# Kernel optimization log

Hardware: AMD Instinct MI355X
Metric: run time of the kernel (lower is better)

## Reference

```python
import jax, jax.numpy as jnp
import numpy as np

NBIT = 8
NSPLIT = 255.0  # 2**NBIT - 1


def _quantized_matmul(x, w_clean, eps):
    # Faithful port of quantization(): bit-slice x into NBIT binary planes, run a
    # noisy linear per plane with weight w + randn*|w|*0.1, and sum. The 8
    # sequential fc() calls are fused into one einsum over the bit axis.
    # x: (..., in); w_clean: (out, in); eps: (NBIT, out, in) standard normal.
    mn = jnp.min(x)
    mx = jnp.max(x)
    q = ((x - mn) / (mx - mn) * NSPLIT).astype(jnp.uint8).astype(jnp.int32)  # truncating cast as in torch
    quant_base = 2 ** jnp.arange(NBIT, dtype=jnp.int32)
    binary = ((q[..., None] & quant_base) != 0).astype(x.dtype)              # (..., in, NBIT)
    scaled = binary * (2.0 ** jnp.arange(NBIT)).astype(x.dtype)              # plane i scaled by 2**i
    w_noisy = w_clean[None] + eps * jnp.abs(w_clean)[None] * 0.1             # (NBIT, out, in)
    z = jnp.einsum('...ib,boi->...o', scaled, w_noisy)
    return z, mn, mx, w_noisy[-1]  # fc.weight after loop == last noisy weight


def _forward(node_embedding, edge_embedding, nbr_mask, cond1, cond2, eps1, eps2, bn_gamma, bn_beta):
    B, At, Nbr, Fe = edge_embedding.shape
    Fn = node_embedding.shape[-1]
    c1 = jnp.concatenate(
        [jnp.broadcast_to(node_embedding[:, :, None, :], (B, At, Nbr, Fn)), edge_embedding],
        axis=3)                                                              # (B, At, Nbr, Fn+Fe)
    # quantization + re_quantization through fc (re-quant uses last noisy fc.weight)
    z1, mn1, mx1, w_last = _quantized_matmul(c1, cond1[0], eps1)
    bias1 = jnp.sum(mn1 * w_last, axis=1)                                    # (H1,)
    h = jax.nn.relu(z1 / NSPLIT * (mx1 - mn1) + bias1)                       # (B, At, Nbr, H1)
    # quantization + re_quantization through fc_2 (re-quant uses conductance[1][-1])
    z2, mn2, mx2, _ = _quantized_matmul(h, cond2[0], eps2)
    bias2 = jnp.sum(mn2 * cond2[-1], axis=1)                                 # (2*Fn,)
    c2 = z2 / NSPLIT * (mx2 - mn2) + bias2                                   # (B, At, Nbr, 2*Fn)
    nbr_gate, nbr_extract = jnp.split(c2, 2, axis=3)
    nbr_sumed = jax.nn.sigmoid(nbr_gate) * jnp.tanh(nbr_extract) * nbr_mask[..., None]
    nbr_sumed = jnp.sum(nbr_sumed, axis=2)                                   # (B, At, Fn)
    # BatchNorm1d in training mode: batch statistics over flattened (B*At)
    flat = nbr_sumed.reshape(-1, Fn)
    mean = jnp.mean(flat, axis=0)
    var = jnp.var(flat, axis=0)  # biased variance, as torch BN uses for normalization
    bn = ((flat - mean) / jnp.sqrt(var + 1e-5) * bn_gamma + bn_beta).reshape(B, At, Fn)
    return jax.nn.relu(node_embedding + bn)


def setup_inputs() -> dict:
    key = jax.random.key(0)
    ks = jax.random.split(key, 7)
    B, At, Nbr, Fn, Fe = 16, 96, 12, 64, 64
    H1, H2 = 4 * (Fn + Fe), 2 * Fn
    return {
        'node_embedding': jax.random.normal(ks[0], (B, At, Fn), jnp.float32),
        'edge_embedding': jax.random.normal(ks[1], (B, At, Nbr, Fe), jnp.float32),
        'nbr_mask': (jax.random.uniform(ks[2], (B, At, Nbr)) > 0.5).astype(jnp.float32),
        'cond1': jax.random.normal(ks[3], (2, H1, Fn + Fe), jnp.float32) * 0.05,
        'cond2': jax.random.normal(ks[4], (2, H2, H1), jnp.float32) * 0.05,
        'eps1': jax.random.normal(ks[5], (NBIT, H1, Fn + Fe), jnp.float32),
        'eps2': jax.random.normal(ks[6], (NBIT, H2, H1), jnp.float32),
        'bn_gamma': jnp.ones((Fn,), jnp.float32),
        'bn_beta': jnp.zeros((Fn,), jnp.float32),
    }


def reference(node_embedding, edge_embedding, nbr_mask, cond1, cond2, eps1, eps2, bn_gamma, bn_beta):
    return _forward(node_embedding, edge_embedding, nbr_mask, cond1, cond2, eps1, eps2, bn_gamma, bn_beta)
```

## Files before the change

### kernel.cpp

```cpp
#include <hip/hip_runtime.h>
#include <stdint.h>

#define B_    16
#define AT_   96
#define NBR_  12
#define FN_   64
#define FE_   64
#define M1    (B_*AT_*NBR_)
#define R_    (B_*AT_)
#define K1Q   128
#define N1    512
#define K2Q   512
#define N2    128
#define SPLIT2 4

typedef _Float16 f16x8 __attribute__((ext_vector_type(8)));
typedef _Float16 f16x2 __attribute__((ext_vector_type(2)));
typedef float    f32x4 __attribute__((ext_vector_type(4)));

#define OFF_SCAL  0u
#define OFF_B1R   256u
#define OFF_B2R   (OFF_B1R + 2048u)
#define OFF_Q1    4096u
#define OFF_W1E   (OFF_Q1  + (size_t)M1*K1Q)
#define OFF_W2E   (OFF_W1E + (size_t)N1*K1Q*8*2)
#define OFF_Q2    (OFF_W2E + (size_t)N2*K2Q*8*2)
#define OFF_H     (OFF_Q2  + (size_t)M1*K2Q)
#define OFF_ZP    OFF_H
#define OFF_NS    (OFF_H   + (size_t)M1*N1*2)

__device__ __forceinline__ unsigned int enc_f(float f) {
    unsigned int u = __float_as_uint(f);
    return (u & 0x80000000u) ? ~u : (u | 0x80000000u);
}
__device__ __forceinline__ float dec_f(unsigned int u) {
    return __uint_as_float((u & 0x80000000u) ? (u & 0x7FFFFFFFu) : ~u);
}

__global__ void k_init(unsigned int* scal, float* b1raw, float* b2raw) {
    int t = threadIdx.x;
    if (t == 0) { scal[0] = 0xFFFFFFFFu; scal[1] = 0u; scal[2] = 0xFFFFFFFFu; scal[3] = 0u; }
    if (t < N1) b1raw[t] = 0.f;
    if (t < N2) b2raw[t] = 0.f;
}

__global__ __launch_bounds__(256) void k_minmax_c1(const float* __restrict__ node,
                                                   const float* __restrict__ edge,
                                                   unsigned int* __restrict__ scal) {
    const int nn4 = (B_*AT_*FN_)/4;
    const int tot4 = nn4 + (M1*FE_)/4;
    float mn = 3.0e38f, mx = -3.0e38f;
    for (int idx = blockIdx.x*blockDim.x + threadIdx.x; idx < tot4; idx += gridDim.x*blockDim.x) {
        float4 x = (idx < nn4) ? ((const float4*)node)[idx] : ((const float4*)edge)[idx - nn4];
        mn = fminf(mn, fminf(fminf(x.x, x.y), fminf(x.z, x.w)));
        mx = fmaxf(mx, fmaxf(fmaxf(x.x, x.y), fmaxf(x.z, x.w)));
    }
    __shared__ float smn[256], smx[256];
    smn[threadIdx.x] = mn; smx[threadIdx.x] = mx; __syncthreads();
    for (int s = 128; s > 0; s >>= 1) {
        if (threadIdx.x < s) {
            smn[threadIdx.x] = fminf(smn[threadIdx.x], smn[threadIdx.x+s]);
            smx[threadIdx.x] = fmaxf(smx[threadIdx.x], smx[threadIdx.x+s]);
        }
        __syncthreads();
    }
    if (threadIdx.x == 0) { atomicMin(&scal[0], enc_f(smn[0])); atomicMax(&scal[1], enc_f(smx[0])); }
}

template<int KQ, int N, int SBASE, bool USE_SECOND>
__global__ __launch_bounds__(256) void k_prep_w16(const float* __restrict__ w_clean,
                                                  const float* __restrict__ eps,
                                                  const unsigned int* __restrict__ scal,
                                                  float* __restrict__ braw,
                                                  _Float16* __restrict__ We) {
    int idx = blockIdx.x*blockDim.x + threadIdx.x;
    if (idx >= N*KQ) return;
    int o = idx / KQ;
    float mn = dec_f(scal[SBASE]), mx = dec_f(scal[SBASE+1]);
    float s = (mx - mn) * (1.0f/255.0f);
    float w = w_clean[idx];
    float aw = fabsf(w) * 0.1f;
    union { _Float16 h[8]; uint4 u; } pk;
    float p = s;
    float v7 = 0.f;
    #pragma unroll
    for (int b = 0; b < 8; b++) {
        float e = eps[(size_t)b*N*KQ + idx];
        float v = w + e*aw;
        if (b == 7) v7 = v;
        pk.h[b] = (_Float16)(v * p);
        p *= 2.0f;
    }
    *(uint4*)&We[(size_t)idx*8] = pk.u;
    float bv = USE_SECOND ? w_clean[(size_t)N*KQ + idx] : v7;
    #pragma unroll
    for (int off = 32; off > 0; off >>= 1) bv += __shfl_down(bv, off);
    if ((threadIdx.x & 63) == 0) atomicAdd(&braw[o], bv);
}

__global__ __launch_bounds__(256) void k_quant_c1(const float* __restrict__ node,
                                                  const float* __restrict__ edge,
                                                  const unsigned int* __restrict__ scal,
                                                  unsigned int* __restrict__ q1) {
    int idx = blockIdx.x*256 + threadIdx.x;
    int m = idx >> 5, dw = idx & 31;
    const float mn = dec_f(scal[0]), rng = dec_f(scal[1]) - mn;
    float4 x;
    if (dw < 16) x = *(const float4*)&node[(m/NBR_)*FN_ + dw*4];
    else         x = *(const float4*)&edge[(size_t)m*FE_ + (dw-16)*4];
    unsigned int b0 = (unsigned char)(int)((x.x - mn) / rng * 255.0f);
    unsigned int b1 = (unsigned char)(int)((x.y - mn) / rng * 255.0f);
    unsigned int b2 = (unsigned char)(int)((x.z - mn) / rng * 255.0f);
    unsigned int b3 = (unsigned char)(int)((x.w - mn) / rng * 255.0f);
    q1[idx] = b0 | (b1 << 8) | (b2 << 16) | (b3 << 24);
}

__global__ __launch_bounds__(256) void k_quant_h(const _Float16* __restrict__ h,
                                                 const unsigned int* __restrict__ scal,
                                                 unsigned int* __restrict__ q2) {
    int idx = blockIdx.x*256 + threadIdx.x;
    const float mn = dec_f(scal[2]), rng = dec_f(scal[3]) - mn;
    f16x8 v = *(const f16x8*)(h + (size_t)idx*8);
    unsigned int lo = 0, hi = 0;
    #pragma unroll
    for (int j = 0; j < 4; j++) {
        float x = (float)v[j];
        lo |= ((unsigned int)(unsigned char)(int)((x - mn) / rng * 255.0f)) << (j*8);
    }
    #pragma unroll
    for (int j = 0; j < 4; j++) {
        float x = (float)v[4+j];
        hi |= ((unsigned int)(unsigned char)(int)((x - mn) / rng * 255.0f)) << (j*8);
    }
    uint2 o; o.x = lo; o.y = hi;
    *(uint2*)&q2[idx*2] = o;
}

__device__ __forceinline__ f16x8 expand_byte(unsigned int byte) {
    unsigned int r2 = byte | (byte << 15);
    union { unsigned int u[4]; f16x8 h; } t;
    t.u[0] = ( r2       & 0x00010001u) * 0x3C00u;
    t.u[1] = ((r2 >> 2) & 0x00010001u) * 0x3C00u;
    t.u[2] = ((r2 >> 4) & 0x00010001u) * 0x3C00u;
    t.u[3] = ((r2 >> 6) & 0x00010001u) * 0x3C00u;
    return t.h;
}

template<int KQ, int N, int SPLITK, bool EPI1>
__global__ __launch_bounds__(256, 3) void kge(const unsigned char* __restrict__ q,
                                              const _Float16* __restrict__ W,
                                              const float* __restrict__ braw,
                                              void* __restrict__ outv,
                                              unsigned int* __restrict__ scal) {
    constexpr int KP  = KQ * 8;
    constexpr int KPS = KP / SPLITK;
    constexpr int NIT = KPS / 64;
    __shared__ __align__(16) unsigned char ldsA[4*64*136];

    const int tid  = threadIdx.x;
    const int lane = tid & 63;
    const int w    = tid >> 6;
    const int l15  = lane & 15;
    const int lq   = lane >> 4;
    const int sh8  = lq * 8;
    const int m0   = blockIdx.x * 256 + w * 64;
    const int o0   = blockIdx.y * 64;
    const int kbase = blockIdx.z * KPS;

    unsigned char* wlds = ldsA + w * (64*136);

    {
        const int rsub = lane >> 3;
        const int c    = lane & 7;
        const unsigned int koff = (unsigned int)(kbase >> 3);
        #pragma unroll
        for (int j = 0; j < 8; ++j) {
            const int row = j*8 + rsub;
            uint4 v = *(const uint4*)(q + (size_t)(m0 + row)*KQ + koff + c*16);
            unsigned char* dst = wlds + row*136 + c*16;
            uint2 lo; lo.x = v.x; lo.y = v.y;
            uint2 hi; hi.x = v.z; hi.y = v.w;
            *(uint2*)dst = lo;
            *(uint2*)(dst + 8) = hi;
        }
    }

    f32x4 acc[4][4] = {};

    unsigned int boff[8];
    #pragma unroll
    for (int nf = 0; nf < 4; ++nf)
        #pragma unroll
        for (int kf = 0; kf < 2; ++kf)
            boff[nf*2+kf] = (unsigned int)(o0 + nf*16 + l15) * KP + kbase + kf*32 + lq*8;

    f16x8 bf0[8], bf1[8];
    #pragma unroll
    for (int j = 0; j < 8; ++j)
        bf0[j] = *(const f16x8*)(W + boff[j]);

    const unsigned char* ards = wlds + l15*136;

    #pragma unroll 2
    for (int it = 0; it < NIT; ++it) {
        const f16x8* cur = (it & 1) ? bf1 : bf0;
        f16x8*       nxt = (it & 1) ? bf0 : bf1;
        if (it + 1 < NIT) {
            #pragma unroll
            for (int j = 0; j < 8; ++j)
                nxt[j] = *(const f16x8*)(W + boff[j] + (it+1)*64);
        }
        uint2 qd[4];
        #pragma unroll
        for (int mf = 0; mf < 4; ++mf)
            qd[mf] = *(const uint2*)(ards + mf*(16*136) + it*8);
        #pragma unroll
        for (int kf = 0; kf < 2; ++kf) {
            #pragma unroll
            for (int mf = 0; mf < 4; ++mf) {
                unsigned int byte = ((kf ? qd[mf].y : qd[mf].x) >> sh8) & 0xFFu;
                f16x8 a = expand_byte(byte);
                #pragma unroll
                for (int nf = 0; nf < 4; ++nf)
                    acc[mf][nf] = __builtin_amdgcn_mfma_f32_16x16x32_f16(a, cur[nf*2+kf], acc[mf][nf], 0, 0, 0);
            }
        }
    }

    if (EPI1) {
        _Float16* out = (_Float16*)outv;
        const float mn1 = dec_f(scal[0]);
        float bv[4];
        #pragma unroll
        for (int nf = 0; nf < 4; ++nf) bv[nf] = mn1 * braw[o0 + nf*16 + l15];
        float tmn = 3.0e38f, tmx = -3.0e38f;
        #pragma unroll
        for (int mf = 0; mf < 4; ++mf) {
            const int mr = m0 + mf*16 + lq*4;
            #pragma unroll
            for (int nf = 0; nf < 4; ++nf) {
                const int oc = o0 + nf*16 + l15;
                #pragma unroll
                for (int r = 0; r < 4; ++r) {
                    float v = fmaxf(acc[mf][nf][r] + bv[nf], 0.0f);
                    _Float16 v16 = (_Float16)v;
                    float vr = (float)v16;
                    tmn = fminf(tmn, vr); tmx = fmaxf(tmx, vr);
                    out[(size_t)(mr + r)*N + oc] = v16;
                }
            }
        }
        float* red = (float*)ldsA;
        __syncthreads();
        red[tid] = tmn; red[256 + tid] = tmx;
        __syncthreads();
        for (int s = 128; s > 0; s >>= 1) {
            if (tid < s) {
                red[tid]       = fminf(red[tid],       red[tid + s]);
                red[256 + tid] = fmaxf(red[256 + tid], red[256 + tid + s]);
            }
            __syncthreads();
        }
        if (tid == 0) { atomicMin(&scal[2], enc_f(red[0])); atomicMax(&scal[3], enc_f(red[256])); }
    } else {
        _Float16* op = (_Float16*)outv + (size_t)blockIdx.z * ((size_t)M1 * N);
        #pragma unroll
        for (int mf = 0; mf < 4; ++mf) {
            const int mr = m0 + mf*16 + lq*4;
            #pragma unroll
            for (int nf = 0; nf < 4; ++nf) {
                const int oc = o0 + nf*16 + l15;
                #pragma unroll
                for (int r = 0; r < 4; ++r)
                    op[(size_t)(mr + r)*N + oc] = (_Float16)acc[mf][nf][r];
            }
        }
    }
}

__global__ __launch_bounds__(256) void k_nbr(const _Float16* __restrict__ zp,
                                             const float* __restrict__ b2raw,
                                             const unsigned int* __restrict__ scal,
                                             const float* __restrict__ mask,
                                             float* __restrict__ ns) {
    const size_t SP = (size_t)M1 * N2;
    int tid = threadIdx.x;
    int r = blockIdx.x*8 + (tid >> 5);
    int f2 = (tid & 31) * 2;
    const float mn2 = dec_f(scal[2]);
    float bg0 = mn2 * b2raw[f2],      bg1 = mn2 * b2raw[f2+1];
    float be0 = mn2 * b2raw[64 + f2], be1 = mn2 * b2raw[65 + f2];
    float s0 = 0.f, s1 = 0.f;
    #pragma unroll
    for (int n = 0; n < NBR_; n++) {
        int m = r*NBR_ + n;
        size_t base = (size_t)m * N2;
        float g0 = bg0, g1 = bg1, e0 = be0, e1 = be1;
        #pragma unroll
        for (int z = 0; z < SPLIT2; z++) {
            f16x2 gv = *(const f16x2*)(zp + z*SP + base + f2);
            f16x2 ev = *(const f16x2*)(zp + z*SP + base + 64 + f2);
            g0 += (float)gv[0]; g1 += (float)gv[1];
            e0 += (float)ev[0]; e1 += (float)ev[1];
        }
        float mk = mask[m];
        s0 += (1.0f / (1.0f + expf(-g0))) * tanhf(e0) * mk;
        s1 += (1.0f / (1.0f + expf(-g1))) * tanhf(e1) * mk;
    }
    float2 o; o.x = s0; o.y = s1;
    *(float2*)&ns[r*64 + f2] = o;
}

__global__ __launch_bounds__(256) void k_bn(const float* __restrict__ ns,
                                            const float* __restrict__ node,
                                            const float* __restrict__ gamma,
                                            const float* __restrict__ beta,
                                            float* __restrict__ out) {
    int f = blockIdx.x;
    int tid = threadIdx.x;
    float x[6];
    float s = 0.f, ss = 0.f;
    #pragma unroll
    for (int k = 0; k < 6; k++) {
        int r = tid + k*256;
        x[k] = ns[r*64 + f];
        s += x[k]; ss += x[k]*x[k];
    }
    __shared__ float rs[256], rss[256];
    rs[tid] = s; rss[tid] = ss; __syncthreads();
    for (int st = 128; st > 0; st >>= 1) {
        if (tid < st) { rs[tid] += rs[tid+st]; rss[tid] += rss[tid+st]; }
        __syncthreads();
    }
    float mean = rs[0] / 1536.0f;
    float var  = rss[0] / 1536.0f - mean*mean;
    float denom = sqrtf(var + 1e-5f);
    float g = gamma[f], bt = beta[f];
    #pragma unroll
    for (int k = 0; k < 6; k++) {
        int r = tid + k*256;
        float v = node[r*64 + f] + ((x[k] - mean) / denom * g + bt);
        out[r*64 + f] = fmaxf(v, 0.f);
    }
}

extern "C" void kernel_launch(void* const* d_in, const int* in_sizes, int n_in,
                              void* d_out, int out_size, void* d_ws, size_t ws_size,
                              hipStream_t stream) {
    const float* node  = (const float*)d_in[0];
    const float* edge  = (const float*)d_in[1];
    const float* mask  = (const float*)d_in[2];
    const float* cond1 = (const float*)d_in[3];
    const float* cond2 = (const float*)d_in[4];
    const float* eps1  = (const float*)d_in[5];
    const float* eps2  = (const float*)d_in[6];
    const float* gamma = (const float*)d_in[7];
    const float* beta  = (const float*)d_in[8];
    float* out = (float*)d_out;
    char* ws = (char*)d_ws;

    unsigned int*  scal = (unsigned int*)(ws + OFF_SCAL);
    float* b1raw = (float*)(ws + OFF_B1R);
    float* b2raw = (float*)(ws + OFF_B2R);
    unsigned char* q1 = (unsigned char*)(ws + OFF_Q1);
    _Float16* W1e = (_Float16*)(ws + OFF_W1E);
    _Float16* W2e = (_Float16*)(ws + OFF_W2E);
    unsigned char* q2 = (unsigned char*)(ws + OFF_Q2);
    _Float16* h  = (_Float16*)(ws + OFF_H);
    _Float16* zp = (_Float16*)(ws + OFF_ZP);
    float*    ns = (float*)(ws + OFF_NS);

    k_init<<<1, 1024, 0, stream>>>(scal, b1raw, b2raw);
    k_minmax_c1<<<512, 256, 0, stream>>>(node, edge, scal);
    k_prep_w16<K1Q, N1, 0, false><<<(N1*K1Q + 255)/256, 256, 0, stream>>>(cond1, eps1, scal, b1raw, W1e);
    k_quant_c1<<<(M1*32)/256, 256, 0, stream>>>(node, edge, scal, (unsigned int*)q1);
    kge<K1Q, N1, 1, true><<<dim3(M1/256, N1/64, 1), 256, 0, stream>>>(q1, W1e, b1raw, h, scal);
    k_prep_w16<K2Q, N2, 2, true><<<(N2*K2Q + 255)/256, 256, 0, stream>>>(cond2, eps2, scal, b2raw, W2e);
    k_quant_h<<<(M1*512/8)/256, 256, 0, stream>>>(h, scal, (unsigned int*)q2);
    kge<K2Q, N2, SPLIT2, false><<<dim3(M1/256, N2/64, SPLIT2), 256, 0, stream>>>(q2, W2e, b2raw, zp, scal);
    k_nbr<<<R_/8, 256, 0, stream>>>(zp, b2raw, scal, mask, ns);
    k_bn<<<64, 256, 0, stream>>>(ns, node, gamma, beta, out);
}
```

Measured before the change: 231.6 us.

## Deepen GEMM weight prefetch to four buffers and remap blocks per XCD

Replaces the two-buffer weight prefetch in the bit-plane GEMM with a four-stage register pipeline that keeps three iterations of B fragments in flight, and software-pipelines the LDS A reads. Block indices are remapped from a flat 1D grid so that consecutive M tiles land on the same XCD, which should improve L2 reuse of the A rows. Launch bounds drop from 3 to 2 waves per SIMD to make room for the larger register footprint, trading occupancy for memory latency hiding. The loop assumes NIT is a multiple of 4.

```diff
diff --git a/kernel.cpp b/kernel.cpp
--- a/kernel.cpp
+++ b/kernel.cpp
@@ -146,8 +146,23 @@
     return t.h;
 }
 
+#define COMPUTE(qd, bf)  do { \
+    _Pragma("unroll") for (int kf = 0; kf < 2; ++kf) { \
+      _Pragma("unroll") for (int mf = 0; mf < 4; ++mf) { \
+        unsigned int byte_ = ((kf ? qd[mf].y : qd[mf].x) >> sh8) & 0xFFu; \
+        f16x8 a_ = expand_byte(byte_); \
+        _Pragma("unroll") for (int nf = 0; nf < 4; ++nf) \
+          acc[mf][nf] = __builtin_amdgcn_mfma_f32_16x16x32_f16(a_, bf[nf*2+kf], acc[mf][nf], 0, 0, 0); \
+      } } } while (0)
+
+#define LOADB(bf, itv) { _Pragma("unroll") for (int jb = 0; jb < 8; ++jb) \
+    bf[jb] = *(const f16x8*)(W + boff[jb] + (unsigned)(itv)*64); }
+
+#define LOADQ(qd, itv) { _Pragma("unroll") for (int mf = 0; mf < 4; ++mf) \
+    qd[mf] = *(const uint2*)(ards + mf*(16*136) + (itv)*8); }
+
 template<int KQ, int N, int SPLITK, bool EPI1>
-__global__ __launch_bounds__(256, 3) void kge(const unsigned char* __restrict__ q,
+__global__ __launch_bounds__(256, 2) void kgh(const unsigned char* __restrict__ q,
                                               const _Float16* __restrict__ W,
                                               const float* __restrict__ braw,
                                               void* __restrict__ outv,
@@ -155,6 +170,9 @@
     constexpr int KP  = KQ * 8;
     constexpr int KPS = KP / SPLITK;
     constexpr int NIT = KPS / 64;
+    constexpr int NOT_ = N / 64;
+    constexpr int MT  = M1 / 256;
+    constexpr int MPX = MT / 8;
     __shared__ __align__(16) unsigned char ldsA[4*64*136];
 
     const int tid  = threadIdx.x;
@@ -163,9 +181,18 @@
     const int l15  = lane & 15;
     const int lq   = lane >> 4;
     const int sh8  = lq * 8;
-    const int m0   = blockIdx.x * 256 + w * 64;
-    const int o0   = blockIdx.y * 64;
-    const int kbase = blockIdx.z * KPS;
+
+    const int lin  = blockIdx.x;
+    const int xcd  = lin & 7;
+    const int jj   = lin >> 3;
+    const int mt   = xcd * MPX + (jj % MPX);
+    const int rest = jj / MPX;
+    const int ot   = rest % NOT_;
+    const int zt   = rest / NOT_;
+
+    const int m0    = mt*256 + w*64;
+    const int o0    = ot*64;
+    const int kbase = zt * KPS;
 
     unsigned char* wlds = ldsA + w * (64*136);
 
@@ -194,37 +221,27 @@
         for (int kf = 0; kf < 2; ++kf)
             boff[nf*2+kf] = (unsigned int)(o0 + nf*16 + l15) * KP + kbase + kf*32 + lq*8;
 
-    f16x8 bf0[8], bf1[8];
-    #pragma unroll
-    for (int j = 0; j < 8; ++j)
-        bf0[j] = *(const f16x8*)(W + boff[j]);
-
     const unsigned char* ards = wlds + l15*136;
 
-    #pragma unroll 2
-    for (int it = 0; it < NIT; ++it) {
-        const f16x8* cur = (it & 1) ? bf1 : bf0;
-        f16x8*       nxt = (it & 1) ? bf0 : bf1;
-        if (it + 1 < NIT) {
-            #pragma unroll
-            for (int j = 0; j < 8; ++j)
-                nxt[j] = *(const f16x8*)(W + boff[j] + (it+1)*64);
-        }
-        uint2 qd[4];
-        #pragma unroll
-        for (int mf = 0; mf < 4; ++mf)
-            qd[mf] = *(const uint2*)(ards + mf*(16*136) + it*8);
-        #pragma unroll
-        for (int kf = 0; kf < 2; ++kf) {
-            #pragma unroll
-            for (int mf = 0; mf < 4; ++mf) {
-                unsigned int byte = ((kf ? qd[mf].y : qd[mf].x) >> sh8) & 0xFFu;
-                f16x8 a = expand_byte(byte);
-                #pragma unroll
-                for (int nf = 0; nf < 4; ++nf)
-                    acc[mf][nf] = __builtin_amdgcn_mfma_f32_16x16x32_f16(a, cur[nf*2+kf], acc[mf][nf], 0, 0, 0);
-            }
-        }
+    f16x8 bufA[8], bufB[8], bufC[8], bufD[8];
+    uint2 qdA[4], qdB[4];
+    LOADB(bufA, 0); LOADB(bufB, 1); LOADB(bufC, 2);
+    LOADQ(qdA, 0);
+
+    #pragma unroll 1
+    for (int it = 0; it < NIT; it += 4) {
+        LOADB(bufD, it+3);
+        LOADQ(qdB, it+1);
+        COMPUTE(qdA, bufA);
+        if (it+4 < NIT) LOADB(bufA, it+4);
+        LOADQ(qdA, it+2);
+        COMPUTE(qdB, bufB);
+        if (it+5 < NIT) LOADB(bufB, it+5);
+        LOADQ(qdB, it+3);
+        COMPUTE(qdA, bufC);
+        if (it+6 < NIT) LOADB(bufC, it+6);
+        if (it+4 < NIT) LOADQ(qdA, it+4);
+        COMPUTE(qdB, bufD);
     }
 
     if (EPI1) {
@@ -263,7 +280,7 @@
         }
         if (tid == 0) { atomicMin(&scal[2], enc_f(red[0])); atomicMax(&scal[3], enc_f(red[256])); }
     } else {
-        _Float16* op = (_Float16*)outv + (size_t)blockIdx.z * ((size_t)M1 * N);
+        _Float16* op = (_Float16*)outv + (size_t)zt * ((size_t)M1 * N);
         #pragma unroll
         for (int mf = 0; mf < 4; ++mf) {
             const int mr = m0 + mf*16 + lq*4;
@@ -374,10 +391,10 @@
     k_minmax_c1<<<512, 256, 0, stream>>>(node, edge, scal);
     k_prep_w16<K1Q, N1, 0, false><<<(N1*K1Q + 255)/256, 256, 0, stream>>>(cond1, eps1, scal, b1raw, W1e);
     k_quant_c1<<<(M1*32)/256, 256, 0, stream>>>(node, edge, scal, (unsigned int*)q1);
-    kge<K1Q, N1, 1, true><<<dim3(M1/256, N1/64, 1), 256, 0, stream>>>(q1, W1e, b1raw, h, scal);
+    kgh<K1Q, N1, 1, true><<<576, 256, 0, stream>>>(q1, W1e, b1raw, h, scal);
     k_prep_w16<K2Q, N2, 2, true><<<(N2*K2Q + 255)/256, 256, 0, stream>>>(cond2, eps2, scal, b2raw, W2e);
     k_quant_h<<<(M1*512/8)/256, 256, 0, stream>>>(h, scal, (unsigned int*)q2);
-    kge<K2Q, N2, SPLIT2, false><<<dim3(M1/256, N2/64, SPLIT2), 256, 0, stream>>>(q2, W2e, b2raw, zp, scal);
+    kgh<K2Q, N2, SPLIT2, false><<<576, 256, 0, stream>>>(q2, W2e, b2raw, zp, scal);
     k_nbr<<<R_/8, 256, 0, stream>>>(zp, b2raw, scal, mask, ns);
     k_bn<<<64, 256, 0, stream>>>(ns, node, gamma, beta, out);
 }
```

Result: no change. 230.9 us (-0.3%).
